# Performance work log

Hardware: AMD Instinct MI355X
Metric: run time of the kernel (lower is better)

The kernel has to match this reference:

```python
import jax, jax.numpy as jnp
import numpy as np

N = 100000      # num_nodes
E = 1600000     # num_edges
F_IN = 128      # node_feature_dim
D_IN = F_IN + 1 # +1 input_cards indicator
H = 128         # hidden dim (both layers)
NUM_CARDS = 110


def _xavier(key, shape):
    fan_out, fan_in = shape
    limit = np.sqrt(6.0 / (fan_in + fan_out))
    return jax.random.uniform(key, shape, jnp.float32, -limit, limit)


def setup_inputs() -> dict:
    key = jax.random.key(0)
    ks = jax.random.split(key, 12)
    x = jax.random.normal(ks[0], (N, F_IN), jnp.float32)
    edge_index = jax.random.randint(ks[1], (2, E), 0, N, jnp.int64)
    input_cards = jax.random.randint(ks[2], (N,), 0, 2, jnp.int32)
    # SAGEConv layer 1: lin_l (neighbors), lin_r (self), each [H, D_IN] + bias
    Wl1 = _xavier(ks[3], (H, D_IN)); bl1 = jnp.zeros((H,), jnp.float32)
    Wr1 = _xavier(ks[4], (H, D_IN)); br1 = jnp.zeros((H,), jnp.float32)
    # SAGEConv layer 2
    Wl2 = _xavier(ks[5], (H, H)); bl2 = jnp.zeros((H,), jnp.float32)
    Wr2 = _xavier(ks[6], (H, H)); br2 = jnp.zeros((H,), jnp.float32)
    # output layer: normal(0, 0.01)
    Wo = 0.01 * jax.random.normal(ks[7], (NUM_CARDS, H), jnp.float32)
    bo = jnp.zeros((NUM_CARDS,), jnp.float32)
    return {"x": x, "Wl1": Wl1, "bl1": bl1, "Wr1": Wr1, "br1": br1,
            "Wl2": Wl2, "bl2": bl2, "Wr2": Wr2, "br2": br2,
            "Wo": Wo, "bo": bo,
            "edge_index": edge_index, "input_cards": input_cards}


def _sage_conv_mean(h, src, dst, deg_inv, Wl, bl, Wr, br):
    # mean-aggregate source-node features at destination nodes
    summed = jax.ops.segment_sum(h[src], dst, num_segments=N)  # [N, d]
    mean = summed * deg_inv[:, None]
    return mean @ Wl.T + bl + h @ Wr.T + br


def reference(x, Wl1, bl1, Wr1, br1, Wl2, bl2, Wr2, br2, Wo, bo,
              edge_index, input_cards):
    src, dst = edge_index[0], edge_index[1]
    deg = jax.ops.segment_sum(jnp.ones((E,), jnp.float32), dst, num_segments=N)
    deg_inv = jnp.where(deg > 0, 1.0 / jnp.maximum(deg, 1.0), 0.0)
    h = jnp.concatenate([x, input_cards.astype(jnp.float32)[:, None]], axis=1)  # [N, D_IN]
    h = jax.nn.relu(_sage_conv_mean(h, src, dst, deg_inv, Wl1, bl1, Wr1, br1))
    h = jax.nn.relu(_sage_conv_mean(h, src, dst, deg_inv, Wl2, bl2, Wr2, br2))
    logits = h @ Wo.T + bo  # [N, NUM_CARDS]
    return logits
```

## Files before the change

kernel.cpp:

```cpp
#include <hip/hip_runtime.h>
#include <hip/hip_bf16.h>

#define N_NODES 100000
#define N_EDGES 1600000
#define HDIM    128
#define KCH     4
#define NUM_CARDS 110
#define NTILES  (N_NODES / 16)
#define GEMM_BLOCKS 1024

#define NB      196
#define MAXB    10240
#define PT      4096
#define PEPT    16

typedef __attribute__((ext_vector_type(8))) short bfrag;
typedef __attribute__((ext_vector_type(4))) float ffrag;
typedef __attribute__((ext_vector_type(2))) float f32x2;

__device__ inline unsigned short f2bf(float f) {
    __hip_bfloat16 h = __float2bfloat16(f);
    unsigned short u; __builtin_memcpy(&u, &h, 2); return u;
}
__device__ inline float bf_lo(unsigned int u) {
    unsigned int v = u << 16; float f; __builtin_memcpy(&f, &v, 4); return f;
}
__device__ inline float bf_hi(unsigned int u) {
    unsigned int v = u & 0xffff0000u; float f; __builtin_memcpy(&f, &v, 4); return f;
}

__device__ inline void gload_lds16(const void* g, void* l) {
    __builtin_amdgcn_global_load_lds(
        (const __attribute__((address_space(1))) unsigned int*)g,
        (__attribute__((address_space(3))) unsigned int*)l, 16, 0, 0);
}


__global__ __launch_bounds__(256) void k_partition(
    const int* __restrict__ src, const int* __restrict__ dst,
    int* __restrict__ bucket_cursor, unsigned int* __restrict__ part) {
    __shared__ int hist[NB];
    __shared__ int hcur[NB];
    const int t = threadIdx.x;
    const int base = blockIdx.x * PT;
    for (int i = t; i < NB; i += 256) hist[i] = 0;
    __syncthreads();
#pragma unroll
    for (int i = 0; i < PEPT; i++) {
        int e = base + i * 256 + t;
        if (e < N_EDGES) atomicAdd(&hist[dst[e] >> 9], 1);
    }
    __syncthreads();
    for (int b = t; b < NB; b += 256) {
        int h = hist[b];
        hcur[b] = h ? atomicAdd(&bucket_cursor[b], h) : 0;
    }
    __syncthreads();
#pragma unroll
    for (int i = 0; i < PEPT; i++) {
        int e = base + i * 256 + t;
        if (e < N_EDGES) {
            int d = dst[e];
            int b = d >> 9;
            int r = atomicAdd(&hcur[b], 1);
            if (r < MAXB)
                part[(size_t)b * MAXB + r] =
                    ((unsigned int)(d & 511) << 17) | (unsigned int)src[e];
        }
    }
}

__global__ __launch_bounds__(256) void k_bucket(
    const unsigned int* __restrict__ part, const int* __restrict__ bucket_cursor,
    int* __restrict__ row_off, int* __restrict__ deg, float* __restrict__ deg_inv,
    int* __restrict__ csr_src) {
    __shared__ int degl[512];
    __shared__ int offl[512];
    __shared__ int curl[512];
    __shared__ int stmp[256];
    const int t = threadIdx.x;
    const int b = blockIdx.x;
    const int n0 = b << 9;
    const int nb = min(512, N_NODES - n0);
    const int cnt = min(bucket_cursor[b], MAXB);
    const int row0 = b * MAXB;
    const unsigned int* pb = &part[(size_t)b * MAXB];

    degl[t] = 0; degl[t + 256] = 0;
    __syncthreads();
    for (int i = t; i < cnt; i += 256)
        atomicAdd(&degl[pb[i] >> 17], 1);
    __syncthreads();
    const int a0 = degl[2 * t], a1 = degl[2 * t + 1];
    stmp[t] = a0 + a1;
    __syncthreads();
    for (int off = 1; off < 256; off <<= 1) {
        int x = (t >= off) ? stmp[t - off] : 0;
        __syncthreads();
        stmp[t] += x;
        __syncthreads();
    }
    const int excl = stmp[t] - (a0 + a1);
    offl[2 * t] = excl;          curl[2 * t] = excl;
    offl[2 * t + 1] = excl + a0; curl[2 * t + 1] = excl + a0;
    __syncthreads();
    for (int i = t; i < nb; i += 256) {
        int n = n0 + i;
        int d = degl[i];
        row_off[n] = row0 + offl[i];
        deg[n] = d;
        deg_inv[n] = (d > 0) ? 1.0f / (float)d : 0.0f;
    }
    for (int i = t; i < cnt; i += 256) {
        unsigned int pk = pb[i];
        int r = atomicAdd(&curl[pk >> 17], 1);
        csr_src[row0 + r] = (int)(pk & 0x1FFFFu);
    }
}


__global__ void k_prep_w(const float* __restrict__ Wl1, const float* __restrict__ Wr1,
                         const float* __restrict__ bl1, const float* __restrict__ br1,
                         const float* __restrict__ Wl2, const float* __restrict__ Wr2,
                         const float* __restrict__ bl2, const float* __restrict__ br2,
                         const float* __restrict__ Wo,  const float* __restrict__ bo,
                         unsigned short* __restrict__ W1, unsigned short* __restrict__ W2,
                         unsigned short* __restrict__ Wob,
                         float* __restrict__ bias1, float* __restrict__ bias2,
                         float* __restrict__ biaso, float* __restrict__ wcard1) {
    const int j = blockIdx.x;
    const int k = threadIdx.x;
    const float* s1 = (j < 128) ? &Wl1[(size_t)j * 129] : &Wr1[(size_t)(j - 128) * 129];
    W1[(size_t)j * HDIM + k] = f2bf(s1[k]);
    const float* s2 = (j < 128) ? &Wl2[(size_t)j * HDIM] : &Wr2[(size_t)(j - 128) * HDIM];
    W2[(size_t)j * HDIM + k] = f2bf(s2[k]);
    if (j < 112)
        Wob[(size_t)j * HDIM + k] = (j < NUM_CARDS) ? f2bf(Wo[(size_t)j * HDIM + k])
                                                    : (unsigned short)0;
    if (k == 0) {
        wcard1[j] = s1[HDIM];
        bias1[j] = (j < 128) ? 0.f : (bl1[j - 128] + br1[j - 128]);
        bias2[j] = (j < 128) ? 0.f : (bl2[j - 128] + br2[j - 128]);
        if (j < 112) biaso[j] = (j < NUM_CARDS) ? bo[j] : 0.f;
    }
}


__global__ __launch_bounds__(256) void k_gemm_dual(
    const unsigned short* __restrict__ Ab, const float* __restrict__ Af,
    const int* __restrict__ cards,
    const unsigned short* __restrict__ W,
    const float* __restrict__ bias, const float* __restrict__ wcard,
    unsigned char* __restrict__ Gq, unsigned short* __restrict__ Rb,
    int layer1) {
    __shared__ __align__(16) unsigned char smem[16384 + 2048];
    float* bias_l = (float*)(smem + 16384);
    float* wc_l   = (float*)(smem + 16384 + 1024);

    const int tix  = threadIdx.x;
    const int wave = tix >> 6;
    const int lane = tix & 63;
    const int m16  = lane & 15;
    const int quad = lane >> 4;
    const int u0   = wave * 4;
    const bool isG = (wave < 2);
    const int xk   = m16 & 7;

    bfrag wf[4][KCH];
#pragma unroll
    for (int u = 0; u < 4; u++) {
        const int j = (u0 + u) * 16 + m16;
#pragma unroll
        for (int c = 0; c < KCH; c++)
            wf[u][c] = *(const bfrag*)&W[(size_t)j * HDIM + c * 32 + quad * 8];
    }

    bias_l[tix] = bias[tix];
    wc_l[tix]   = layer1 ? wcard[tix] : 0.f;

    const int sw1 = (tix ^ ((tix >> 5) & 7)) << 4;
    const int sw2 = (tix ^ ((tix >> 4) & 7)) << 4;
    const int ldsoff = wave << 10;

    int tile = blockIdx.x;
    if (layer1) {
        const unsigned char* g = (const unsigned char*)Af + (size_t)tile * 8192;
        gload_lds16(g + sw1,        smem + ldsoff);
        gload_lds16(g + sw1 + 4096, smem + 4096 + ldsoff);
    } else {
        const unsigned char* g = (const unsigned char*)Ab + (size_t)tile * 4096;
        gload_lds16(g + sw2, smem + ldsoff);
    }
    float cvn = layer1 ? (float)cards[tile * 16 + m16] : 0.f;
    __syncthreads();

    for (int buf = 0; tile < NTILES; tile += GEMM_BLOCKS, buf ^= 1) {
        const int tn = tile + GEMM_BLOCKS;
        const bool more = (tn < NTILES);
        const float cv = cvn;

        if (more) {
            if (layer1) {
                const unsigned char* g = (const unsigned char*)Af + (size_t)tn * 8192;
                unsigned char* d = smem + (buf ^ 1) * 8192 + ldsoff;
                gload_lds16(g + sw1,        d);
                gload_lds16(g + sw1 + 4096, d + 4096);
                cvn = (float)cards[tn * 16 + m16];
            } else {
                const unsigned char* g = (const unsigned char*)Ab + (size_t)tn * 4096;
                gload_lds16(g + sw2, smem + (buf ^ 1) * 4096 + ldsoff);
            }
        }

        const unsigned char* B = smem + buf * (layer1 ? 8192 : 4096);
        bfrag hf[KCH];
        if (layer1) {
#pragma unroll
            for (int c = 0; c < KCH; c++) {
                const int s0 = m16 * 32 + c * 8 + quad * 2;
                const float4 p0 = *(const float4*)(B + (((s0    ) ^ xk) << 4));
                const float4 p1 = *(const float4*)(B + (((s0 + 1) ^ xk) << 4));
                bfrag h;
                h[0] = (short)f2bf(p0.x); h[1] = (short)f2bf(p0.y);
                h[2] = (short)f2bf(p0.z); h[3] = (short)f2bf(p0.w);
                h[4] = (short)f2bf(p1.x); h[5] = (short)f2bf(p1.y);
                h[6] = (short)f2bf(p1.z); h[7] = (short)f2bf(p1.w);
                hf[c] = h;
            }
        } else {
#pragma unroll
            for (int c = 0; c < KCH; c++) {
                const int s = m16 * 16 + c * 4 + quad;
                hf[c] = *(const bfrag*)(B + ((s ^ xk) << 4));
            }
        }

        const int node = tile * 16 + m16;
#pragma unroll
        for (int u = 0; u < 4; u++) {
            ffrag acc = {0.f, 0.f, 0.f, 0.f};
#pragma unroll
            for (int c = 0; c < KCH; c++)
                acc = __builtin_amdgcn_mfma_f32_16x16x32_bf16(wf[u][c], hf[c], acc, 0, 0, 0);
            const int jj0 = (u0 + u) * 16 + quad * 4;
            const float4 b0 = *(const float4*)&bias_l[jj0];
            const float4 w0 = *(const float4*)&wc_l[jj0];
            float v[4];
            v[0] = acc[0] + b0.x + cv * w0.x;
            v[1] = acc[1] + b0.y + cv * w0.y;
            v[2] = acc[2] + b0.z + cv * w0.z;
            v[3] = acc[3] + b0.w + cv * w0.w;
            if (isG) {
                int pk = __builtin_amdgcn_cvt_pk_fp8_f32(v[0], v[1], 0, false);
                pk = __builtin_amdgcn_cvt_pk_fp8_f32(v[2], v[3], pk, true);
                *(unsigned int*)&Gq[(size_t)node * HDIM + (u0 + u) * 16 + quad * 4] =
                    (unsigned int)pk;
            } else {
                unsigned short o[4];
#pragma unroll
                for (int r = 0; r < 4; r++) o[r] = f2bf(v[r]);
                uint2 p = {(unsigned int)o[0] | ((unsigned int)o[1] << 16),
                           (unsigned int)o[2] | ((unsigned int)o[3] << 16)};
                *(uint2*)&Rb[(size_t)node * HDIM + (u0 + u - 8) * 16 + quad * 4] = p;
            }
        }

        if (more) __syncthreads();
    }
}


__global__ __launch_bounds__(256) void k_agg(
    const unsigned char* __restrict__ Gq, const unsigned short* __restrict__ Rb,
    const int* __restrict__ row_off, const int* __restrict__ deg,
    const float* __restrict__ deg_inv, const int* __restrict__ csr_src,
    unsigned short* __restrict__ outH) {
    const int wave = threadIdx.x >> 6;
    const int lane = threadIdx.x & 63;
    const int g = lane >> 3;
    const int l = lane & 7;
    const int n = (blockIdx.x * 4 + wave) * 8 + g;
    const int start = row_off[n];
    const int d = deg[n];
    const float di = deg_inv[n];
    const int fo = l * 16;

    int dmax = d;
    dmax = max(dmax, __shfl_xor(dmax, 8, 64));
    dmax = max(dmax, __shfl_xor(dmax, 16, 64));
    dmax = max(dmax, __shfl_xor(dmax, 32, 64));

    const uint4 rv0 = *(const uint4*)&Rb[(size_t)n * HDIM + fo];
    const uint4 rv1 = *(const uint4*)&Rb[(size_t)n * HDIM + fo + 8];

    f32x2 acc2[8];
#pragma unroll
    for (int i = 0; i < 8; i++) acc2[i] = (f32x2){0.f, 0.f};

    int idxA = (l < d) ? csr_src[start + l] * HDIM : 0;
    int idxB = (8 + l < d) ? csr_src[start + 8 + l] * HDIM : 0;

    uint4 cur = {0u, 0u, 0u, 0u};
    {
        const int off0 = __shfl(idxA, g << 3, 64);
        if (0 < d) cur = *(const uint4*)&Gq[(size_t)(unsigned)off0 + fo];
    }
#define ACC16(Cv)                                                        \
    acc2[0] += __builtin_amdgcn_cvt_pk_f32_fp8((int)(Cv).x, false);      \
    acc2[1] += __builtin_amdgcn_cvt_pk_f32_fp8((int)(Cv).x, true);       \
    acc2[2] += __builtin_amdgcn_cvt_pk_f32_fp8((int)(Cv).y, false);      \
    acc2[3] += __builtin_amdgcn_cvt_pk_f32_fp8((int)(Cv).y, true);       \
    acc2[4] += __builtin_amdgcn_cvt_pk_f32_fp8((int)(Cv).z, false);      \
    acc2[5] += __builtin_amdgcn_cvt_pk_f32_fp8((int)(Cv).z, true);       \
    acc2[6] += __builtin_amdgcn_cvt_pk_f32_fp8((int)(Cv).w, false);      \
    acc2[7] += __builtin_amdgcn_cvt_pk_f32_fp8((int)(Cv).w, true);

    for (int i = 1; i < dmax; i++) {
        const int sl = i & 7;
        if (sl == 0) {
            idxA = idxB;
            const int j = i + 8 + l;
            idxB = (j < d) ? csr_src[start + j] * HDIM : 0;
        }
        const int offn = __shfl(idxA, (g << 3) | sl, 64);
        uint4 nxt = {0u, 0u, 0u, 0u};
        if (i < d) nxt = *(const uint4*)&Gq[(size_t)(unsigned)offn + fo];
        ACC16(cur);
        cur = nxt;
    }
    ACC16(cur);
#undef ACC16

    const float r[16] = {bf_lo(rv0.x), bf_hi(rv0.x), bf_lo(rv0.y), bf_hi(rv0.y),
                         bf_lo(rv0.z), bf_hi(rv0.z), bf_lo(rv0.w), bf_hi(rv0.w),
                         bf_lo(rv1.x), bf_hi(rv1.x), bf_lo(rv1.y), bf_hi(rv1.y),
                         bf_lo(rv1.z), bf_hi(rv1.z), bf_lo(rv1.w), bf_hi(rv1.w)};
    unsigned short o[16];
#pragma unroll
    for (int i = 0; i < 8; i++) {
        o[2 * i]     = f2bf(fmaxf(acc2[i].x * di + r[2 * i], 0.f));
        o[2 * i + 1] = f2bf(fmaxf(acc2[i].y * di + r[2 * i + 1], 0.f));
    }
    uint4 p0, p1;
    p0.x = (unsigned int)o[0] | ((unsigned int)o[1] << 16);
    p0.y = (unsigned int)o[2] | ((unsigned int)o[3] << 16);
    p0.z = (unsigned int)o[4] | ((unsigned int)o[5] << 16);
    p0.w = (unsigned int)o[6] | ((unsigned int)o[7] << 16);
    p1.x = (unsigned int)o[8] | ((unsigned int)o[9] << 16);
    p1.y = (unsigned int)o[10] | ((unsigned int)o[11] << 16);
    p1.z = (unsigned int)o[12] | ((unsigned int)o[13] << 16);
    p1.w = (unsigned int)o[14] | ((unsigned int)o[15] << 16);
    *(uint4*)&outH[(size_t)n * HDIM + fo] = p0;
    *(uint4*)&outH[(size_t)n * HDIM + fo + 8] = p1;
}


__global__ __launch_bounds__(256) void k_gemm_logits(
    const unsigned short* __restrict__ A, const unsigned short* __restrict__ W,
    const float* __restrict__ bias, float* __restrict__ out) {
    __shared__ __align__(16) unsigned char smem[8192];
    const int tix  = threadIdx.x;
    const int wave = tix >> 6;
    const int lane = tix & 63;
    const int m16  = lane & 15;
    const int quad = lane >> 4;
    const int u0   = wave * 2;
    const int xk   = m16 & 7;

    bfrag wf[2][KCH];
    float bsj[2];
#pragma unroll
    for (int u = 0; u < 2; u++) {
        const int unit = u0 + u;
        const int j = (unit < 7 ? unit : 0) * 16 + m16;
#pragma unroll
        for (int c = 0; c < KCH; c++)
            wf[u][c] = *(const bfrag*)&W[(size_t)j * HDIM + c * 32 + quad * 8];
        bsj[u] = bias[j];
    }

    const int sw2 = (tix ^ ((tix >> 4) & 7)) << 4;
    const int ldsoff = wave << 10;

    int tile = blockIdx.x;
    {
        const unsigned char* g = (const unsigned char*)A + (size_t)tile * 4096;
        gload_lds16(g + sw2, smem + ldsoff);
    }
    __syncthreads();

    for (int buf = 0; tile < NTILES; tile += GEMM_BLOCKS, buf ^= 1) {
        const int tn = tile + GEMM_BLOCKS;
        const bool more = (tn < NTILES);
        if (more) {
            const unsigned char* g = (const unsigned char*)A + (size_t)tn * 4096;
            gload_lds16(g + sw2, smem + (buf ^ 1) * 4096 + ldsoff);
        }

        const unsigned char* B = smem + buf * 4096;
        bfrag hf[KCH];
#pragma unroll
        for (int c = 0; c < KCH; c++) {
            const int s = m16 * 16 + c * 4 + quad;
            hf[c] = *(const bfrag*)(B + ((s ^ xk) << 4));
        }

#pragma unroll
        for (int u = 0; u < 2; u++) {
            const int unit = u0 + u;
            if (unit >= 7) break;
            ffrag acc = {0.f, 0.f, 0.f, 0.f};
#pragma unroll
            for (int c = 0; c < KCH; c++)
                acc = __builtin_amdgcn_mfma_f32_16x16x32_bf16(hf[c], wf[u][c], acc, 0, 0, 0);
            const int j = unit * 16 + m16;
            if (j < NUM_CARDS) {
#pragma unroll
                for (int r = 0; r < 4; r++) {
                    const int node = tile * 16 + quad * 4 + r;
                    out[(size_t)node * NUM_CARDS + j] = acc[r] + bsj[u];
                }
            }
        }

        if (more) __syncthreads();
    }
}


static inline size_t align_up(size_t x, size_t a) { return (x + a - 1) & ~(a - 1); }

extern "C" void kernel_launch(void* const* d_in, const int* in_sizes, int n_in,
                              void* d_out, int out_size, void* d_ws, size_t ws_size,
                              hipStream_t stream) {
    const float* x   = (const float*)d_in[0];
    const float* Wl1 = (const float*)d_in[1];
    const float* bl1 = (const float*)d_in[2];
    const float* Wr1 = (const float*)d_in[3];
    const float* br1 = (const float*)d_in[4];
    const float* Wl2 = (const float*)d_in[5];
    const float* bl2 = (const float*)d_in[6];
    const float* Wr2 = (const float*)d_in[7];
    const float* br2 = (const float*)d_in[8];
    const float* Wo  = (const float*)d_in[9];
    const float* bo  = (const float*)d_in[10];
    const int* edge  = (const int*)d_in[11];
    const int* cards = (const int*)d_in[12];
    float* logits = (float*)d_out;

    const int* e_src = edge;
    const int* e_dst = edge + N_EDGES;

    char* w = (char*)d_ws;
    size_t off = 0;
    int* bucket_cursor = (int*)(w + off); off = align_up(off + 256 * 4, 512);
    unsigned int* part = (unsigned int*)(w + off); off = align_up(off + (size_t)NB * MAXB * 4, 512);
    int* row_off = (int*)(w + off); off = align_up(off + N_NODES * 4, 512);
    int* deg_i   = (int*)(w + off); off = align_up(off + N_NODES * 4, 512);
    float* dinv  = (float*)(w + off); off = align_up(off + N_NODES * 4, 512);
    int* csr_src = (int*)(w + off); off = align_up(off + (size_t)NB * MAXB * 4, 512);
    unsigned char*  Gq   = (unsigned char*)(w + off);  off = align_up(off + (size_t)N_NODES * HDIM, 512);
    unsigned short* Rb   = (unsigned short*)(w + off); off = align_up(off + (size_t)N_NODES * HDIM * 2, 512);
    unsigned short* bufH = (unsigned short*)(w + off); off = align_up(off + (size_t)N_NODES * HDIM * 2, 512);
    unsigned short* W1   = (unsigned short*)(w + off); off = align_up(off + 256 * HDIM * 2, 512);
    unsigned short* W2   = (unsigned short*)(w + off); off = align_up(off + 256 * HDIM * 2, 512);
    unsigned short* Wob  = (unsigned short*)(w + off); off = align_up(off + 112 * HDIM * 2, 512);
    float* bias1  = (float*)(w + off); off = align_up(off + 256 * 4, 512);
    float* bias2  = (float*)(w + off); off = align_up(off + 256 * 4, 512);
    float* biaso  = (float*)(w + off); off = align_up(off + 112 * 4, 512);
    float* wcard1 = (float*)(w + off); off = align_up(off + 256 * 4, 512);
    (void)ws_size; (void)n_in; (void)in_sizes; (void)out_size;

    hipMemsetAsync(bucket_cursor, 0, 256 * 4, stream);
    k_prep_w<<<256, 128, 0, stream>>>(Wl1, Wr1, bl1, br1, Wl2, Wr2, bl2, br2, Wo, bo,
                                      W1, W2, Wob, bias1, bias2, biaso, wcard1);

    const int PBLK = (N_EDGES + PT - 1) / PT;
    k_partition<<<PBLK, 256, 0, stream>>>(e_src, e_dst, bucket_cursor, part);
    k_bucket<<<NB, 256, 0, stream>>>(part, bucket_cursor,
                                     row_off, deg_i, dinv, csr_src);

    k_gemm_dual<<<GEMM_BLOCKS, 256, 0, stream>>>(nullptr, x, cards, W1, bias1, wcard1, Gq, Rb, 1);
    k_agg<<<N_NODES / 32, 256, 0, stream>>>(Gq, Rb, row_off, deg_i, dinv, csr_src, bufH);
    k_gemm_dual<<<GEMM_BLOCKS, 256, 0, stream>>>(bufH, nullptr, nullptr, W2, bias2, wcard1, Gq, Rb, 0);
    k_agg<<<N_NODES / 32, 256, 0, stream>>>(Gq, Rb, row_off, deg_i, dinv, csr_src, bufH);
    k_gemm_logits<<<GEMM_BLOCKS, 256, 0, stream>>>(bufH, Wob, biaso, logits);
}
```

Before: 317.4 us.

## Triple-buffer GEMM tiles with single barrier and batch gather loads in aggregation

The GEMM kernels move from double-buffered LDS staging with two __syncthreads per tile to a three-slot ring. Each tile now uses a partial vmcnt wait and one s_barrier, and layer 1 vs 2 becomes a template parameter. The aggregation kernel replaces its one-ahead gather loop with chunks of eight independent fp8 row loads, prefetching the next chunk while the current one is consumed, to keep more memory requests in flight. The cost is more LDS per block and more registers for the gather queues, which could reduce occupancy. It also relies on hand-counted waitcnt values being correct.

```diff
diff --git a/kernel.cpp b/kernel.cpp
--- a/kernel.cpp
+++ b/kernel.cpp
@@ -146,16 +146,17 @@
 }
 
 
+template <int L1>
 __global__ __launch_bounds__(256) void k_gemm_dual(
     const unsigned short* __restrict__ Ab, const float* __restrict__ Af,
     const int* __restrict__ cards,
     const unsigned short* __restrict__ W,
     const float* __restrict__ bias, const float* __restrict__ wcard,
-    unsigned char* __restrict__ Gq, unsigned short* __restrict__ Rb,
-    int layer1) {
-    __shared__ __align__(16) unsigned char smem[16384 + 2048];
-    float* bias_l = (float*)(smem + 16384);
-    float* wc_l   = (float*)(smem + 16384 + 1024);
+    unsigned char* __restrict__ Gq, unsigned short* __restrict__ Rb) {
+    constexpr int BUFSZ = L1 ? 8192 : 4096;
+    __shared__ __align__(16) unsigned char smem[3 * BUFSZ + 2048];
+    float* bias_l = (float*)(smem + 3 * BUFSZ);
+    float* wc_l   = (float*)(smem + 3 * BUFSZ + 1024);
 
     const int tix  = threadIdx.x;
     const int wave = tix >> 6;
@@ -176,45 +177,51 @@
     }
 
     bias_l[tix] = bias[tix];
-    wc_l[tix]   = layer1 ? wcard[tix] : 0.f;
-
-    const int sw1 = (tix ^ ((tix >> 5) & 7)) << 4;
-    const int sw2 = (tix ^ ((tix >> 4) & 7)) << 4;
+    wc_l[tix]   = L1 ? wcard[tix] : 0.f;
+
+    const int sw = L1 ? ((tix ^ ((tix >> 5) & 7)) << 4)
+                      : ((tix ^ ((tix >> 4) & 7)) << 4);
     const int ldsoff = wave << 10;
 
+    int rawc = 0, rawc_n = 0;
+
+#define STAGE_DUAL(T, BI)                                                     \
+    do {                                                                      \
+        unsigned char* dst_ = smem + (BI) * BUFSZ + ldsoff;                   \
+        if (L1) {                                                             \
+            rawc_n = cards[(T) * 16 + m16];                                   \
+            const unsigned char* g_ =                                         \
+                (const unsigned char*)Af + (size_t)(T) * 8192;                \
+            gload_lds16(g_ + sw, dst_);                                       \
+            gload_lds16(g_ + sw + 4096, dst_ + 4096);                         \
+        } else {                                                              \
+            const unsigned char* g_ =                                         \
+                (const unsigned char*)Ab + (size_t)(T) * 4096;                \
+            gload_lds16(g_ + sw, dst_);                                       \
+        }                                                                     \
+    } while (0)
+
     int tile = blockIdx.x;
-    if (layer1) {
-        const unsigned char* g = (const unsigned char*)Af + (size_t)tile * 8192;
-        gload_lds16(g + sw1,        smem + ldsoff);
-        gload_lds16(g + sw1 + 4096, smem + 4096 + ldsoff);
-    } else {
-        const unsigned char* g = (const unsigned char*)Ab + (size_t)tile * 4096;
-        gload_lds16(g + sw2, smem + ldsoff);
-    }
-    float cvn = layer1 ? (float)cards[tile * 16 + m16] : 0.f;
-    __syncthreads();
-
-    for (int buf = 0; tile < NTILES; tile += GEMM_BLOCKS, buf ^= 1) {
+    STAGE_DUAL(tile, 0);
+    rawc = rawc_n;
+    asm volatile("s_waitcnt lgkmcnt(0)" ::: "memory");
+
+    int b = 0;
+    for (; tile < NTILES; tile += GEMM_BLOCKS) {
         const int tn = tile + GEMM_BLOCKS;
-        const bool more = (tn < NTILES);
-        const float cv = cvn;
-
-        if (more) {
-            if (layer1) {
-                const unsigned char* g = (const unsigned char*)Af + (size_t)tn * 8192;
-                unsigned char* d = smem + (buf ^ 1) * 8192 + ldsoff;
-                gload_lds16(g + sw1,        d);
-                gload_lds16(g + sw1 + 4096, d + 4096);
-                cvn = (float)cards[tn * 16 + m16];
-            } else {
-                const unsigned char* g = (const unsigned char*)Ab + (size_t)tn * 4096;
-                gload_lds16(g + sw2, smem + (buf ^ 1) * 4096 + ldsoff);
-            }
-        }
-
-        const unsigned char* B = smem + buf * (layer1 ? 8192 : 4096);
+        const float cv = L1 ? (float)rawc : 0.f;
+        if (tn < NTILES) {
+            STAGE_DUAL(tn, (b == 2 ? 0 : b + 1));
+            rawc = rawc_n;
+        }
+        if (L1) asm volatile("s_waitcnt vmcnt(3)" ::: "memory");
+        else    asm volatile("s_waitcnt vmcnt(1)" ::: "memory");
+        __builtin_amdgcn_s_barrier();
+        __builtin_amdgcn_sched_barrier(0);
+
+        const unsigned char* B = smem + b * BUFSZ;
         bfrag hf[KCH];
-        if (layer1) {
+        if (L1) {
 #pragma unroll
             for (int c = 0; c < KCH; c++) {
                 const int s0 = m16 * 32 + c * 8 + quad * 2;
@@ -264,9 +271,9 @@
                 *(uint2*)&Rb[(size_t)node * HDIM + (u0 + u - 8) * 16 + quad * 4] = p;
             }
         }
-
-        if (more) __syncthreads();
-    }
+        b = (b == 2 ? 0 : b + 1);
+    }
+#undef STAGE_DUAL
 }
 
 
@@ -297,14 +304,11 @@
 #pragma unroll
     for (int i = 0; i < 8; i++) acc2[i] = (f32x2){0.f, 0.f};
 
-    int idxA = (l < d) ? csr_src[start + l] * HDIM : 0;
-    int idxB = (8 + l < d) ? csr_src[start + 8 + l] * HDIM : 0;
-
-    uint4 cur = {0u, 0u, 0u, 0u};
-    {
-        const int off0 = __shfl(idxA, g << 3, 64);
-        if (0 < d) cur = *(const uint4*)&Gq[(size_t)(unsigned)off0 + fo];
-    }
+    const int i0 = (l      < d) ? csr_src[start + l     ] * HDIM : 0;
+    const int i1 = (l + 8  < d) ? csr_src[start + l +  8] * HDIM : 0;
+    const int i2 = (l + 16 < d) ? csr_src[start + l + 16] * HDIM : 0;
+    const int i3 = (l + 24 < d) ? csr_src[start + l + 24] * HDIM : 0;
+
 #define ACC16(Cv)                                                        \
     acc2[0] += __builtin_amdgcn_cvt_pk_f32_fp8((int)(Cv).x, false);      \
     acc2[1] += __builtin_amdgcn_cvt_pk_f32_fp8((int)(Cv).x, true);       \
@@ -315,20 +319,45 @@
     acc2[6] += __builtin_amdgcn_cvt_pk_f32_fp8((int)(Cv).w, false);      \
     acc2[7] += __builtin_amdgcn_cvt_pk_f32_fp8((int)(Cv).w, true);
 
-    for (int i = 1; i < dmax; i++) {
-        const int sl = i & 7;
-        if (sl == 0) {
-            idxA = idxB;
-            const int j = i + 8 + l;
-            idxB = (j < d) ? csr_src[start + j] * HDIM : 0;
-        }
-        const int offn = __shfl(idxA, (g << 3) | sl, 64);
-        uint4 nxt = {0u, 0u, 0u, 0u};
-        if (i < d) nxt = *(const uint4*)&Gq[(size_t)(unsigned)offn + fo];
-        ACC16(cur);
-        cur = nxt;
-    }
-    ACC16(cur);
+#define LOADCHUNK(Q, IR, CB)                                                  \
+    {                                                                         \
+        _Pragma("unroll")                                                     \
+        for (int k = 0; k < 8; k++) {                                         \
+            const int off_ = __shfl((IR), (g << 3) | k, 64);                  \
+            uint4 t_ = {0u, 0u, 0u, 0u};                                      \
+            if ((CB) + k < d)                                                 \
+                t_ = *(const uint4*)&Gq[(size_t)(unsigned)off_ + fo];         \
+            Q[k] = t_;                                                        \
+        }                                                                     \
+    }
+#define CONSUME(Q)                                                            \
+    {                                                                         \
+        _Pragma("unroll")                                                     \
+        for (int k = 0; k < 8; k++) { ACC16(Q[k]); }                          \
+    }
+
+    uint4 qa[8], qb[8];
+    const bool m1 = dmax > 8, m2 = dmax > 16, m3 = dmax > 24;
+
+    LOADCHUNK(qa, i0, 0)
+    if (m1) LOADCHUNK(qb, i1, 8)
+    CONSUME(qa)
+    if (m2) LOADCHUNK(qa, i2, 16)
+    if (m1) CONSUME(qb)
+    if (m3) LOADCHUNK(qb, i3, 24)
+    if (m2) CONSUME(qa)
+    if (m3) CONSUME(qb)
+
+    if (dmax > 32) {
+        for (int c = 4; c * 8 < dmax; c++) {
+            const int jj = c * 8 + l;
+            const int ir = (jj < d) ? csr_src[start + jj] * HDIM : 0;
+            LOADCHUNK(qa, ir, c * 8)
+            CONSUME(qa)
+        }
+    }
+#undef LOADCHUNK
+#undef CONSUME
 #undef ACC16
 
     const float r[16] = {bf_lo(rv0.x), bf_hi(rv0.x), bf_lo(rv0.y), bf_hi(rv0.y),
@@ -358,7 +387,7 @@
 __global__ __launch_bounds__(256) void k_gemm_logits(
     const unsigned short* __restrict__ A, const unsigned short* __restrict__ W,
     const float* __restrict__ bias, float* __restrict__ out) {
-    __shared__ __align__(16) unsigned char smem[8192];
+    __shared__ __align__(16) unsigned char smem[3 * 4096];
     const int tix  = threadIdx.x;
     const int wave = tix >> 6;
     const int lane = tix & 63;
@@ -387,17 +416,19 @@
         const unsigned char* g = (const unsigned char*)A + (size_t)tile * 4096;
         gload_lds16(g + sw2, smem + ldsoff);
     }
-    __syncthreads();
-
-    for (int buf = 0; tile < NTILES; tile += GEMM_BLOCKS, buf ^= 1) {
+
+    int b = 0;
+    for (; tile < NTILES; tile += GEMM_BLOCKS) {
         const int tn = tile + GEMM_BLOCKS;
-        const bool more = (tn < NTILES);
-        if (more) {
+        if (tn < NTILES) {
             const unsigned char* g = (const unsigned char*)A + (size_t)tn * 4096;
-            gload_lds16(g + sw2, smem + (buf ^ 1) * 4096 + ldsoff);
-        }
-
-        const unsigned char* B = smem + buf * 4096;
+            gload_lds16(g + sw2, smem + (b == 2 ? 0 : b + 1) * 4096 + ldsoff);
+        }
+        asm volatile("s_waitcnt vmcnt(1)" ::: "memory");
+        __builtin_amdgcn_s_barrier();
+        __builtin_amdgcn_sched_barrier(0);
+
+        const unsigned char* B = smem + b * 4096;
         bfrag hf[KCH];
 #pragma unroll
         for (int c = 0; c < KCH; c++) {
@@ -422,8 +453,7 @@
                 }
             }
         }
-
-        if (more) __syncthreads();
+        b = (b == 2 ? 0 : b + 1);
     }
 }
 
@@ -480,9 +510,9 @@
     k_bucket<<<NB, 256, 0, stream>>>(part, bucket_cursor,
                                      row_off, deg_i, dinv, csr_src);
 
-    k_gemm_dual<<<GEMM_BLOCKS, 256, 0, stream>>>(nullptr, x, cards, W1, bias1, wcard1, Gq, Rb, 1);
+    k_gemm_dual<1><<<GEMM_BLOCKS, 256, 0, stream>>>(nullptr, x, cards, W1, bias1, wcard1, Gq, Rb);
     k_agg<<<N_NODES / 32, 256, 0, stream>>>(Gq, Rb, row_off, deg_i, dinv, csr_src, bufH);
-    k_gemm_dual<<<GEMM_BLOCKS, 256, 0, stream>>>(bufH, nullptr, nullptr, W2, bias2, wcard1, Gq, Rb, 0);
+    k_gemm_dual<0><<<GEMM_BLOCKS, 256, 0, stream>>>(bufH, nullptr, nullptr, W2, bias2, wcard1, Gq, Rb);
     k_agg<<<N_NODES / 32, 256, 0, stream>>>(Gq, Rb, row_off, deg_i, dinv, csr_src, bufH);
     k_gemm_logits<<<GEMM_BLOCKS, 256, 0, stream>>>(bufH, Wob, biaso, logits);
 }
```

Result: no change. 313.4 us (-1.2%).

## Fuse aggregation with following GEMMs and triple-buffer layer-1 GEMM loads

Applied to the files above, without the earlier changes.

Each aggregation kernel now keeps its 32 aggregated node rows in LDS and immediately runs the next layer's GEMM (layer-2 projection or output logits), so the bf16 hidden buffer is never written to and re-read from global memory. That removes two kernel launches and the round trip through global memory. The layer-1 GEMM becomes a dedicated kernel with a 3-stage LDS pipeline, explicit vmcnt waits and card values preloaded into LDS. In exchange, the fused kernels reload weight fragments per 32-node block instead of once per persistent block, and they need separate Gq2/Rb2 buffers.

```diff
diff --git a/kernel.cpp b/kernel.cpp
--- a/kernel.cpp
+++ b/kernel.cpp
@@ -21,12 +21,6 @@
 __device__ inline unsigned short f2bf(float f) {
     __hip_bfloat16 h = __float2bfloat16(f);
     unsigned short u; __builtin_memcpy(&u, &h, 2); return u;
-}
-__device__ inline float bf_lo(unsigned int u) {
-    unsigned int v = u << 16; float f; __builtin_memcpy(&f, &v, 4); return f;
-}
-__device__ inline float bf_hi(unsigned int u) {
-    unsigned int v = u & 0xffff0000u; float f; __builtin_memcpy(&f, &v, 4); return f;
 }
 
 __device__ inline void gload_lds16(const void* g, void* l) {
@@ -146,16 +140,15 @@
 }
 
 
-__global__ __launch_bounds__(256) void k_gemm_dual(
-    const unsigned short* __restrict__ Ab, const float* __restrict__ Af,
-    const int* __restrict__ cards,
+__global__ __launch_bounds__(256) void k_gemm1(
+    const float* __restrict__ Af, const int* __restrict__ cards,
     const unsigned short* __restrict__ W,
     const float* __restrict__ bias, const float* __restrict__ wcard,
-    unsigned char* __restrict__ Gq, unsigned short* __restrict__ Rb,
-    int layer1) {
-    __shared__ __align__(16) unsigned char smem[16384 + 2048];
-    float* bias_l = (float*)(smem + 16384);
-    float* wc_l   = (float*)(smem + 16384 + 1024);
+    unsigned char* __restrict__ Gq, unsigned short* __restrict__ Rb) {
+    __shared__ __align__(16) unsigned char smem[3 * 8192 + 2048 + 512];
+    float* bias_l = (float*)(smem + 3 * 8192);
+    float* wc_l   = (float*)(smem + 3 * 8192 + 1024);
+    float* cl     = (float*)(smem + 3 * 8192 + 2048);
 
     const int tix  = threadIdx.x;
     const int wave = tix >> 6;
@@ -165,6 +158,7 @@
     const int u0   = wave * 4;
     const bool isG = (wave < 2);
     const int xk   = m16 & 7;
+    const int bid  = blockIdx.x;
 
     bfrag wf[4][KCH];
 #pragma unroll
@@ -176,63 +170,53 @@
     }
 
     bias_l[tix] = bias[tix];
-    wc_l[tix]   = layer1 ? wcard[tix] : 0.f;
-
-    const int sw1 = (tix ^ ((tix >> 5) & 7)) << 4;
-    const int sw2 = (tix ^ ((tix >> 4) & 7)) << 4;
+    wc_l[tix]   = wcard[tix];
+    if (tix < 16) {
+#pragma unroll
+        for (int i = 0; i < 7; i++) {
+            const int t = bid + i * GEMM_BLOCKS;
+            if (t < NTILES) cl[i * 16 + tix] = (float)cards[t * 16 + tix];
+        }
+    }
+
+    const int sw = (tix ^ ((tix >> 5) & 7)) << 4;
     const int ldsoff = wave << 10;
 
+#define STAGE1(T, BI)                                                         \
+    do {                                                                      \
+        const unsigned char* g_ = (const unsigned char*)Af + (size_t)(T) * 8192; \
+        unsigned char* d_ = smem + (BI) * 8192 + ldsoff;                      \
+        gload_lds16(g_ + sw, d_);                                             \
+        gload_lds16(g_ + sw + 4096, d_ + 4096);                               \
+    } while (0)
+
     int tile = blockIdx.x;
-    if (layer1) {
-        const unsigned char* g = (const unsigned char*)Af + (size_t)tile * 8192;
-        gload_lds16(g + sw1,        smem + ldsoff);
-        gload_lds16(g + sw1 + 4096, smem + 4096 + ldsoff);
-    } else {
-        const unsigned char* g = (const unsigned char*)Ab + (size_t)tile * 4096;
-        gload_lds16(g + sw2, smem + ldsoff);
-    }
-    float cvn = layer1 ? (float)cards[tile * 16 + m16] : 0.f;
-    __syncthreads();
-
-    for (int buf = 0; tile < NTILES; tile += GEMM_BLOCKS, buf ^= 1) {
+    STAGE1(tile, 0);
+    asm volatile("s_waitcnt lgkmcnt(0)" ::: "memory");
+
+    int b = 0, ic = 0;
+    for (; tile < NTILES; tile += GEMM_BLOCKS, ic++) {
         const int tn = tile + GEMM_BLOCKS;
-        const bool more = (tn < NTILES);
-        const float cv = cvn;
-
-        if (more) {
-            if (layer1) {
-                const unsigned char* g = (const unsigned char*)Af + (size_t)tn * 8192;
-                unsigned char* d = smem + (buf ^ 1) * 8192 + ldsoff;
-                gload_lds16(g + sw1,        d);
-                gload_lds16(g + sw1 + 4096, d + 4096);
-                cvn = (float)cards[tn * 16 + m16];
-            } else {
-                const unsigned char* g = (const unsigned char*)Ab + (size_t)tn * 4096;
-                gload_lds16(g + sw2, smem + (buf ^ 1) * 4096 + ldsoff);
-            }
-        }
-
-        const unsigned char* B = smem + buf * (layer1 ? 8192 : 4096);
+        if (tn < NTILES) STAGE1(tn, (b == 2 ? 0 : b + 1));
+        asm volatile("s_waitcnt vmcnt(2)" ::: "memory");
+        __builtin_amdgcn_s_barrier();
+        __builtin_amdgcn_sched_barrier(0);
+
+        const float cv = cl[ic * 16 + m16];
+
+        const unsigned char* B = smem + b * 8192;
         bfrag hf[KCH];
-        if (layer1) {
-#pragma unroll
-            for (int c = 0; c < KCH; c++) {
-                const int s0 = m16 * 32 + c * 8 + quad * 2;
-                const float4 p0 = *(const float4*)(B + (((s0    ) ^ xk) << 4));
-                const float4 p1 = *(const float4*)(B + (((s0 + 1) ^ xk) << 4));
-                bfrag h;
-                h[0] = (short)f2bf(p0.x); h[1] = (short)f2bf(p0.y);
-                h[2] = (short)f2bf(p0.z); h[3] = (short)f2bf(p0.w);
-                h[4] = (short)f2bf(p1.x); h[5] = (short)f2bf(p1.y);
-                h[6] = (short)f2bf(p1.z); h[7] = (short)f2bf(p1.w);
-                hf[c] = h;
-            }
-        } else {
-#pragma unroll
-            for (int c = 0; c < KCH; c++) {
-                const int s = m16 * 16 + c * 4 + quad;
-                hf[c] = *(const bfrag*)(B + ((s ^ xk) << 4));
-            }
+#pragma unroll
+        for (int c = 0; c < KCH; c++) {
+            const int s0 = m16 * 32 + c * 8 + quad * 2;
+            const float4 p0 = *(const float4*)(B + (((s0    ) ^ xk) << 4));
+            const float4 p1 = *(const float4*)(B + (((s0 + 1) ^ xk) << 4));
+            bfrag h;
+            h[0] = (short)f2bf(p0.x); h[1] = (short)f2bf(p0.y);
+            h[2] = (short)f2bf(p0.z); h[3] = (short)f2bf(p0.w);
+            h[4] = (short)f2bf(p1.x); h[5] = (short)f2bf(p1.y);
+            h[6] = (short)f2bf(p1.z); h[7] = (short)f2bf(p1.w);
+            hf[c] = h;
         }
 
         const int node = tile * 16 + m16;
@@ -264,47 +248,56 @@
                 *(uint2*)&Rb[(size_t)node * HDIM + (u0 + u - 8) * 16 + quad * 4] = p;
             }
         }
-
-        if (more) __syncthreads();
-    }
-}
-
-
-__global__ __launch_bounds__(256) void k_agg(
+        b = (b == 2 ? 0 : b + 1);
+    }
+#undef STAGE1
+}
+
+
+template <int MODE>
+__global__ __launch_bounds__(256) void k_agg_gemm(
     const unsigned char* __restrict__ Gq, const unsigned short* __restrict__ Rb,
     const int* __restrict__ row_off, const int* __restrict__ deg,
     const float* __restrict__ deg_inv, const int* __restrict__ csr_src,
-    unsigned short* __restrict__ outH) {
-    const int wave = threadIdx.x >> 6;
-    const int lane = threadIdx.x & 63;
-    const int g = lane >> 3;
-    const int l = lane & 7;
-    const int n = (blockIdx.x * 4 + wave) * 8 + g;
-    const int start = row_off[n];
-    const int d = deg[n];
-    const float di = deg_inv[n];
-    const int fo = l * 16;
-
-    int dmax = d;
-    dmax = max(dmax, __shfl_xor(dmax, 8, 64));
-    dmax = max(dmax, __shfl_xor(dmax, 16, 64));
-    dmax = max(dmax, __shfl_xor(dmax, 32, 64));
-
-    const uint4 rv0 = *(const uint4*)&Rb[(size_t)n * HDIM + fo];
-    const uint4 rv1 = *(const uint4*)&Rb[(size_t)n * HDIM + fo + 8];
-
-    f32x2 acc2[8];
-#pragma unroll
-    for (int i = 0; i < 8; i++) acc2[i] = (f32x2){0.f, 0.f};
-
-    int idxA = (l < d) ? csr_src[start + l] * HDIM : 0;
-    int idxB = (8 + l < d) ? csr_src[start + 8 + l] * HDIM : 0;
-
-    uint4 cur = {0u, 0u, 0u, 0u};
+    const unsigned short* __restrict__ W, const float* __restrict__ bias,
+    unsigned char* __restrict__ Gq2, unsigned short* __restrict__ Rb2,
+    float* __restrict__ out) {
+    __shared__ __align__(16) unsigned char hlds[32 * 256];
+
+    const int tix  = threadIdx.x;
+    const int wave = tix >> 6;
+    const int lane = tix & 63;
+
     {
-        const int off0 = __shfl(idxA, g << 3, 64);
-        if (0 < d) cur = *(const uint4*)&Gq[(size_t)(unsigned)off0 + fo];
-    }
+        const int g = lane >> 3;
+        const int l = lane & 7;
+        const int nl = wave * 8 + g;
+        const int n = blockIdx.x * 32 + nl;
+        const int start = row_off[n];
+        const int d = deg[n];
+        const float di = deg_inv[n];
+        const int fo = l * 16;
+
+        int dmax = d;
+        dmax = max(dmax, __shfl_xor(dmax, 8, 64));
+        dmax = max(dmax, __shfl_xor(dmax, 16, 64));
+        dmax = max(dmax, __shfl_xor(dmax, 32, 64));
+
+        const uint4 rv0 = *(const uint4*)&Rb[(size_t)n * HDIM + fo];
+        const uint4 rv1 = *(const uint4*)&Rb[(size_t)n * HDIM + fo + 8];
+
+        f32x2 acc2[8];
+#pragma unroll
+        for (int i = 0; i < 8; i++) acc2[i] = (f32x2){0.f, 0.f};
+
+        int idxA = (l < d) ? csr_src[start + l] * HDIM : 0;
+        int idxB = (8 + l < d) ? csr_src[start + 8 + l] * HDIM : 0;
+
+        uint4 cur = {0u, 0u, 0u, 0u};
+        {
+            const int off0 = __shfl(idxA, g << 3, 64);
+            if (0 < d) cur = *(const uint4*)&Gq[(size_t)(unsigned)off0 + fo];
+        }
 #define ACC16(Cv)                                                        \
     acc2[0] += __builtin_amdgcn_cvt_pk_f32_fp8((int)(Cv).x, false);      \
     acc2[1] += __builtin_amdgcn_cvt_pk_f32_fp8((int)(Cv).x, true);       \
@@ -315,115 +308,133 @@
     acc2[6] += __builtin_amdgcn_cvt_pk_f32_fp8((int)(Cv).w, false);      \
     acc2[7] += __builtin_amdgcn_cvt_pk_f32_fp8((int)(Cv).w, true);
 
-    for (int i = 1; i < dmax; i++) {
-        const int sl = i & 7;
-        if (sl == 0) {
-            idxA = idxB;
-            const int j = i + 8 + l;
-            idxB = (j < d) ? csr_src[start + j] * HDIM : 0;
-        }
-        const int offn = __shfl(idxA, (g << 3) | sl, 64);
-        uint4 nxt = {0u, 0u, 0u, 0u};
-        if (i < d) nxt = *(const uint4*)&Gq[(size_t)(unsigned)offn + fo];
+        for (int i = 1; i < dmax; i++) {
+            const int sl = i & 7;
+            if (sl == 0) {
+                idxA = idxB;
+                const int j = i + 8 + l;
+                idxB = (j < d) ? csr_src[start + j] * HDIM : 0;
+            }
+            const int offn = __shfl(idxA, (g << 3) | sl, 64);
+            uint4 nxt = {0u, 0u, 0u, 0u};
+            if (i < d) nxt = *(const uint4*)&Gq[(size_t)(unsigned)offn + fo];
+            ACC16(cur);
+            cur = nxt;
+        }
         ACC16(cur);
-        cur = nxt;
-    }
-    ACC16(cur);
 #undef ACC16
 
-    const float r[16] = {bf_lo(rv0.x), bf_hi(rv0.x), bf_lo(rv0.y), bf_hi(rv0.y),
-                         bf_lo(rv0.z), bf_hi(rv0.z), bf_lo(rv0.w), bf_hi(rv0.w),
-                         bf_lo(rv1.x), bf_hi(rv1.x), bf_lo(rv1.y), bf_hi(rv1.y),
-                         bf_lo(rv1.z), bf_hi(rv1.z), bf_lo(rv1.w), bf_hi(rv1.w)};
-    unsigned short o[16];
-#pragma unroll
-    for (int i = 0; i < 8; i++) {
-        o[2 * i]     = f2bf(fmaxf(acc2[i].x * di + r[2 * i], 0.f));
-        o[2 * i + 1] = f2bf(fmaxf(acc2[i].y * di + r[2 * i + 1], 0.f));
-    }
-    uint4 p0, p1;
-    p0.x = (unsigned int)o[0] | ((unsigned int)o[1] << 16);
-    p0.y = (unsigned int)o[2] | ((unsigned int)o[3] << 16);
-    p0.z = (unsigned int)o[4] | ((unsigned int)o[5] << 16);
-    p0.w = (unsigned int)o[6] | ((unsigned int)o[7] << 16);
-    p1.x = (unsigned int)o[8] | ((unsigned int)o[9] << 16);
-    p1.y = (unsigned int)o[10] | ((unsigned int)o[11] << 16);
-    p1.z = (unsigned int)o[12] | ((unsigned int)o[13] << 16);
-    p1.w = (unsigned int)o[14] | ((unsigned int)o[15] << 16);
-    *(uint4*)&outH[(size_t)n * HDIM + fo] = p0;
-    *(uint4*)&outH[(size_t)n * HDIM + fo + 8] = p1;
-}
-
-
-__global__ __launch_bounds__(256) void k_gemm_logits(
-    const unsigned short* __restrict__ A, const unsigned short* __restrict__ W,
-    const float* __restrict__ bias, float* __restrict__ out) {
-    __shared__ __align__(16) unsigned char smem[8192];
-    const int tix  = threadIdx.x;
-    const int wave = tix >> 6;
-    const int lane = tix & 63;
+        const unsigned int ru[8] = {rv0.x, rv0.y, rv0.z, rv0.w,
+                                    rv1.x, rv1.y, rv1.z, rv1.w};
+        unsigned short o[16];
+#pragma unroll
+        for (int i = 0; i < 8; i++) {
+            unsigned int lo_ = ru[i] << 16, hi_ = ru[i] & 0xffff0000u;
+            float rl, rh;
+            __builtin_memcpy(&rl, &lo_, 4); __builtin_memcpy(&rh, &hi_, 4);
+            o[2 * i]     = f2bf(fmaxf(acc2[i].x * di + rl, 0.f));
+            o[2 * i + 1] = f2bf(fmaxf(acc2[i].y * di + rh, 0.f));
+        }
+        uint4 p0, p1;
+        p0.x = (unsigned int)o[0] | ((unsigned int)o[1] << 16);
+        p0.y = (unsigned int)o[2] | ((unsigned int)o[3] << 16);
+        p0.z = (unsigned int)o[4] | ((unsigned int)o[5] << 16);
+        p0.w = (unsigned int)o[6] | ((unsigned int)o[7] << 16);
+        p1.x = (unsigned int)o[8] | ((unsigned int)o[9] << 16);
+        p1.y = (unsigned int)o[10] | ((unsigned int)o[11] << 16);
+        p1.z = (unsigned int)o[12] | ((unsigned int)o[13] << 16);
+        p1.w = (unsigned int)o[14] | ((unsigned int)o[15] << 16);
+        *(uint4*)(hlds + nl * 256 + (((l * 2    ) ^ g) << 4)) = p0;
+        *(uint4*)(hlds + nl * 256 + (((l * 2 + 1) ^ g) << 4)) = p1;
+    }
+    __syncthreads();
+    __builtin_amdgcn_sched_barrier(0);
+
     const int m16  = lane & 15;
     const int quad = lane >> 4;
-    const int u0   = wave * 2;
     const int xk   = m16 & 7;
 
-    bfrag wf[2][KCH];
-    float bsj[2];
-#pragma unroll
-    for (int u = 0; u < 2; u++) {
-        const int unit = u0 + u;
-        const int j = (unit < 7 ? unit : 0) * 16 + m16;
-#pragma unroll
-        for (int c = 0; c < KCH; c++)
-            wf[u][c] = *(const bfrag*)&W[(size_t)j * HDIM + c * 32 + quad * 8];
-        bsj[u] = bias[j];
-    }
-
-    const int sw2 = (tix ^ ((tix >> 4) & 7)) << 4;
-    const int ldsoff = wave << 10;
-
-    int tile = blockIdx.x;
-    {
-        const unsigned char* g = (const unsigned char*)A + (size_t)tile * 4096;
-        gload_lds16(g + sw2, smem + ldsoff);
-    }
-    __syncthreads();
-
-    for (int buf = 0; tile < NTILES; tile += GEMM_BLOCKS, buf ^= 1) {
-        const int tn = tile + GEMM_BLOCKS;
-        const bool more = (tn < NTILES);
-        if (more) {
-            const unsigned char* g = (const unsigned char*)A + (size_t)tn * 4096;
-            gload_lds16(g + sw2, smem + (buf ^ 1) * 4096 + ldsoff);
-        }
-
-        const unsigned char* B = smem + buf * 4096;
-        bfrag hf[KCH];
+    bfrag hf[2][KCH];
+#pragma unroll
+    for (int T = 0; T < 2; T++)
 #pragma unroll
         for (int c = 0; c < KCH; c++) {
-            const int s = m16 * 16 + c * 4 + quad;
-            hf[c] = *(const bfrag*)(B + ((s ^ xk) << 4));
-        }
-
+            const int chunk = (c * 4 + quad) ^ xk;
+            hf[T][c] = *(const bfrag*)(hlds + (T * 16 + m16) * 256 + (chunk << 4));
+        }
+
+    if (MODE == 0) {
+        const int u0 = wave * 4;
+        const bool isG = (wave < 2);
+        bfrag wf[4][KCH];
+#pragma unroll
+        for (int u = 0; u < 4; u++) {
+            const int j = (u0 + u) * 16 + m16;
+#pragma unroll
+            for (int c = 0; c < KCH; c++)
+                wf[u][c] = *(const bfrag*)&W[(size_t)j * HDIM + c * 32 + quad * 8];
+        }
+#pragma unroll
+        for (int T = 0; T < 2; T++) {
+            const int node = blockIdx.x * 32 + T * 16 + m16;
+#pragma unroll
+            for (int u = 0; u < 4; u++) {
+                ffrag acc = {0.f, 0.f, 0.f, 0.f};
+#pragma unroll
+                for (int c = 0; c < KCH; c++)
+                    acc = __builtin_amdgcn_mfma_f32_16x16x32_bf16(wf[u][c], hf[T][c], acc, 0, 0, 0);
+                const int jj0 = (u0 + u) * 16 + quad * 4;
+                const float4 b0 = *(const float4*)&bias[jj0];
+                float v[4] = {acc[0] + b0.x, acc[1] + b0.y,
+                              acc[2] + b0.z, acc[3] + b0.w};
+                if (isG) {
+                    int pk = __builtin_amdgcn_cvt_pk_fp8_f32(v[0], v[1], 0, false);
+                    pk = __builtin_amdgcn_cvt_pk_fp8_f32(v[2], v[3], pk, true);
+                    *(unsigned int*)&Gq2[(size_t)node * HDIM + (u0 + u) * 16 + quad * 4] =
+                        (unsigned int)pk;
+                } else {
+                    unsigned short oo[4];
+#pragma unroll
+                    for (int r = 0; r < 4; r++) oo[r] = f2bf(v[r]);
+                    uint2 p = {(unsigned int)oo[0] | ((unsigned int)oo[1] << 16),
+                               (unsigned int)oo[2] | ((unsigned int)oo[3] << 16)};
+                    *(uint2*)&Rb2[(size_t)node * HDIM + (u0 + u - 8) * 16 + quad * 4] = p;
+                }
+            }
+        }
+    } else {
+        const int u0 = wave * 2;
+        bfrag wf[2][KCH];
+        float bsj[2];
 #pragma unroll
         for (int u = 0; u < 2; u++) {
             const int unit = u0 + u;
-            if (unit >= 7) break;
-            ffrag acc = {0.f, 0.f, 0.f, 0.f};
+            const int j = (unit < 7 ? unit : 0) * 16 + m16;
 #pragma unroll
             for (int c = 0; c < KCH; c++)
-                acc = __builtin_amdgcn_mfma_f32_16x16x32_bf16(hf[c], wf[u][c], acc, 0, 0, 0);
-            const int j = unit * 16 + m16;
-            if (j < NUM_CARDS) {
-#pragma unroll
-                for (int r = 0; r < 4; r++) {
-                    const int node = tile * 16 + quad * 4 + r;
-                    out[(size_t)node * NUM_CARDS + j] = acc[r] + bsj[u];
+                wf[u][c] = *(const bfrag*)&W[(size_t)j * HDIM + c * 32 + quad * 8];
+            bsj[u] = bias[j];
+        }
+#pragma unroll
+        for (int T = 0; T < 2; T++) {
+#pragma unroll
+            for (int u = 0; u < 2; u++) {
+                const int unit = u0 + u;
+                if (unit >= 7) break;
+                ffrag acc = {0.f, 0.f, 0.f, 0.f};
+#pragma unroll
+                for (int c = 0; c < KCH; c++)
+                    acc = __builtin_amdgcn_mfma_f32_16x16x32_bf16(hf[T][c], wf[u][c], acc, 0, 0, 0);
+                const int j = unit * 16 + m16;
+                if (j < NUM_CARDS) {
+#pragma unroll
+                    for (int r = 0; r < 4; r++) {
+                        const int node = blockIdx.x * 32 + T * 16 + quad * 4 + r;
+                        out[(size_t)node * NUM_CARDS + j] = acc[r] + bsj[u];
+                    }
                 }
             }
         }
-
-        if (more) __syncthreads();
     }
 }
 
@@ -461,7 +472,8 @@
     int* csr_src = (int*)(w + off); off = align_up(off + (size_t)NB * MAXB * 4, 512);
     unsigned char*  Gq   = (unsigned char*)(w + off);  off = align_up(off + (size_t)N_NODES * HDIM, 512);
     unsigned short* Rb   = (unsigned short*)(w + off); off = align_up(off + (size_t)N_NODES * HDIM * 2, 512);
-    unsigned short* bufH = (unsigned short*)(w + off); off = align_up(off + (size_t)N_NODES * HDIM * 2, 512);
+    unsigned char*  Gq2  = (unsigned char*)(w + off);  off = align_up(off + (size_t)N_NODES * HDIM, 512);
+    unsigned short* Rb2  = (unsigned short*)(w + off); off = align_up(off + (size_t)N_NODES * HDIM * 2, 512);
     unsigned short* W1   = (unsigned short*)(w + off); off = align_up(off + 256 * HDIM * 2, 512);
     unsigned short* W2   = (unsigned short*)(w + off); off = align_up(off + 256 * HDIM * 2, 512);
     unsigned short* Wob  = (unsigned short*)(w + off); off = align_up(off + 112 * HDIM * 2, 512);
@@ -480,9 +492,9 @@
     k_bucket<<<NB, 256, 0, stream>>>(part, bucket_cursor,
                                      row_off, deg_i, dinv, csr_src);
 
-    k_gemm_dual<<<GEMM_BLOCKS, 256, 0, stream>>>(nullptr, x, cards, W1, bias1, wcard1, Gq, Rb, 1);
-    k_agg<<<N_NODES / 32, 256, 0, stream>>>(Gq, Rb, row_off, deg_i, dinv, csr_src, bufH);
-    k_gemm_dual<<<GEMM_BLOCKS, 256, 0, stream>>>(bufH, nullptr, nullptr, W2, bias2, wcard1, Gq, Rb, 0);
-    k_agg<<<N_NODES / 32, 256, 0, stream>>>(Gq, Rb, row_off, deg_i, dinv, csr_src, bufH);
-    k_gemm_logits<<<GEMM_BLOCKS, 256, 0, stream>>>(bufH, Wob, biaso, logits);
-}
+    k_gemm1<<<GEMM_BLOCKS, 256, 0, stream>>>(x, cards, W1, bias1, wcard1, Gq, Rb);
+    k_agg_gemm<0><<<N_NODES / 32, 256, 0, stream>>>(
+        Gq, Rb, row_off, deg_i, dinv, csr_src, W2, bias2, Gq2, Rb2, nullptr);
+    k_agg_gemm<1><<<N_NODES / 32, 256, 0, stream>>>(
+        Gq2, Rb2, row_off, deg_i, dinv, csr_src, Wob, biaso, nullptr, nullptr, logits);
+}
```

New measurement: 347.0 us. +9.3%, slower.
